# Optimization experiments

Measured on AMD Instinct MI355X. Metric: run time of the kernel, lower is better.

## Reference

```python
import jax, jax.numpy as jnp
import numpy as np

N_HEADS = 16
MAX_REL = 64  # max_relative_pos_len


def setup_inputs() -> dict:
    key = jax.random.key(0)
    ks = jax.random.split(key, 8)
    B, S, D = 2, 2048, 1024
    d = D // N_HEADS
    sc = 0.02
    return {
        "hidden_states": jax.random.normal(ks[0], (B, S, D), jnp.float32),
        "attention_mask": jnp.zeros((B, 1, 1, S), jnp.float32),
        "Wq": jax.random.normal(ks[1], (D, D), jnp.float32) * sc,
        "bq": jnp.zeros((D,), jnp.float32),
        "Wk": jax.random.normal(ks[2], (D, D), jnp.float32) * sc,
        "bk": jnp.zeros((D,), jnp.float32),
        "Wv": jax.random.normal(ks[3], (D, D), jnp.float32) * sc,
        "bv": jnp.zeros((D,), jnp.float32),
        "emb_k": jax.random.normal(ks[4], (2 * MAX_REL + 1, d), jnp.float32) * sc,
        "emb_v": jax.random.normal(ks[5], (2 * MAX_REL + 1, d), jnp.float32) * sc,
    }


def reference(hidden_states, attention_mask, Wq, bq, Wk, bk, Wv, bv, emb_k, emb_v):
    B, S, D = hidden_states.shape
    H = N_HEADS
    d = D // H
    scale = 1.0 / jnp.sqrt(jnp.asarray(d, hidden_states.dtype))

    def heads(x):  # [B,S,D] -> [B,H,S,d]
        return x.reshape(B, S, H, d).transpose(0, 2, 1, 3)

    q = heads(hidden_states @ Wq + bq)
    k = heads(hidden_states @ Wk + bk)
    v = heads(hidden_states @ Wv + bv)

    # relative position indices, clamped: [S_q, S_k]
    rel_idx = jnp.clip(jnp.arange(S)[:, None] - jnp.arange(S)[None, :], -MAX_REL, MAX_REL) + MAX_REL
    rel_k = emb_k[rel_idx]  # [S, S, d]

    # content scores + relative-key bias, both scaled by 1/sqrt(d)
    scores = (jnp.einsum('bhqd,bhkd->bhqk', q, k)
              + jnp.einsum('bhqd,qkd->bhqk', q, rel_k)) * scale
    scores = scores + attention_mask
    probs = jax.nn.softmax(scores, axis=-1)  # dropout is identity at p=0

    rel_v = emb_v[rel_idx]  # [S, S, d]
    ctx = (jnp.einsum('bhqk,bhkd->bhqd', probs, v)
           + jnp.einsum('bhqk,qkd->bhqd', probs, rel_v))
    return ctx.transpose(0, 2, 1, 3).reshape(B, S, D)
```

## Files before the change

kernel.cpp:

```cpp
#include <hip/hip_runtime.h>
#include <stdint.h>

typedef unsigned short u16;
typedef __attribute__((ext_vector_type(8))) short short8;
typedef __attribute__((ext_vector_type(4))) short s16x4;
typedef __attribute__((ext_vector_type(4))) float f32x4;
typedef __attribute__((ext_vector_type(4))) unsigned short u16x4;

#define S_LEN 2048
#define NH 16
#define DMODEL 1024
#define NR 129
#define LOG2E 1.44269504f

#define MFMA(a,b,c) __builtin_amdgcn_mfma_f32_16x16x32_bf16((a),(b),(c),0,0,0)

__device__ __forceinline__ u16 f2bf(float f){
  uint32_t u = __float_as_uint(f);
  u += 0x7fff + ((u >> 16) & 1);
  return (u16)(u >> 16);
}
__device__ __forceinline__ u16 f2bfa(float f){
  return (u16)((__float_as_uint(f) + 0x8000u) >> 16);
}
__device__ __forceinline__ float bf2f(u16 h){ return __uint_as_float(((uint32_t)h) << 16); }

__device__ __forceinline__ uint32_t cvtpk(float lo, float hi){
  uint32_t r;
  asm("v_cvt_pk_bf16_f32 %0, %1, %2" : "=v"(r) : "v"(lo), "v"(hi));
  return r;
}

__device__ __forceinline__ void gl_lds16(const u16* g, u16* l){
  __builtin_amdgcn_global_load_lds((const __attribute__((address_space(1))) void*)g,
                                   (__attribute__((address_space(3))) void*)l, 16, 0, 0);
}

__global__ __launch_bounds__(256) void k_prep(const float* __restrict__ X,
                                              const float* __restrict__ Wq, const float* __restrict__ Wk,
                                              const float* __restrict__ Wv, const float* __restrict__ Wemb,
                                              const float* __restrict__ mask,
                                              u16* __restrict__ Xb, u16* __restrict__ Wt,
                                              u16* __restrict__ Eb, float* __restrict__ maskL){
  const int bid = blockIdx.x, tid = threadIdx.x;
  if (bid < 4096){
    int i = bid * 256 + tid;
    const float4* xp = (const float4*)X;
    float4 v = xp[i];
    u16x4 o; o.x = f2bf(v.x); o.y = f2bf(v.y); o.z = f2bf(v.z); o.w = f2bf(v.w);
    *(u16x4*)(Xb + (size_t)i * 4) = o;
  } else if (bid < 4864){
    int b2 = bid - 4096;
    int z = b2 >> 8;
    const float* W = (z == 0) ? Wq : (z == 1) ? Wk : Wv;
    u16* Ot = Wt + (size_t)z * 1024 * 1024;
    __shared__ float t[64][65];
    int k0 = ((b2 >> 4) & 15) * 64, n0 = (b2 & 15) * 64;
    int c = tid & 63, r0 = (tid >> 6) * 16;
    #pragma unroll
    for (int i = 0; i < 16; ++i) t[r0 + i][c] = W[(size_t)(k0 + r0 + i) * 1024 + n0 + c];
    __syncthreads();
    #pragma unroll
    for (int i = 0; i < 16; ++i) Ot[(size_t)(n0 + r0 + i) * 1024 + k0 + c] = f2bf(t[c][r0 + i]);
  } else if (bid < 4900){
    int idx = (bid - 4864) * 256 + tid;
    if (idx < 144 * 64){
      int r = idx >> 6;
      Eb[idx] = (r < NR) ? f2bf(Wemb[idx]) : (u16)0;
    }
  } else {
    int idx = (bid - 4900) * 256 + tid;
    maskL[idx] = mask[idx] * LOG2E;
  }
}

__global__ __launch_bounds__(256) void k_qkv(const u16* __restrict__ Xb, const u16* __restrict__ Wt,
                                             const float* __restrict__ bq, const float* __restrict__ bk,
                                             const float* __restrict__ bv,
                                             u16* __restrict__ Qs, u16* __restrict__ Kb, u16* __restrict__ Vb){
  const int z = blockIdx.z;
  const u16* W = Wt + (size_t)z * 1024 * 1024;
  const float* bias = (z == 0) ? bq : (z == 1) ? bk : bv;
  u16* outp = (z == 0) ? Qs : (z == 1) ? Kb : Vb;
  const float vs = (z == 0) ? 0.125f * LOG2E : 1.0f;
  const int n0 = blockIdx.x * 128, m0 = blockIdx.y * 128;
  const int tid = threadIdx.x, w = tid >> 6, lane = tid & 63, l15 = lane & 15, quad = lane >> 4;
  const int wm = (w >> 1) * 64, wn = (w & 1) * 64;
  __shared__ __attribute__((aligned(16))) u16 As[128 * 32];
  __shared__ __attribute__((aligned(16))) u16 Bs[128 * 32];
  f32x4 acc[4][4];
  #pragma unroll
  for (int i = 0; i < 4; ++i)
    #pragma unroll
    for (int j = 0; j < 4; ++j) acc[i][j] = (f32x4){0.f,0.f,0.f,0.f};

  const int rA = lane >> 2, cA = (lane & 3) * 8;
  const u16* aBase = Xb + (size_t)(m0 + w * 16 + rA) * 1024 + cA;
  const u16* bBase = W  + (size_t)(n0 + w * 16 + rA) * 1024 + cA;
  u16* aDst0 = As + (w * 16) * 32;  u16* aDst1 = As + (64 + w * 16) * 32;
  u16* bDst0 = Bs + (w * 16) * 32;  u16* bDst1 = Bs + (64 + w * 16) * 32;

  for (int k0 = 0; k0 < 1024; k0 += 32){
    __syncthreads();
    gl_lds16(aBase + k0,             aDst0);
    gl_lds16(aBase + 64 * 1024 + k0, aDst1);
    gl_lds16(bBase + k0,             bDst0);
    gl_lds16(bBase + 64 * 1024 + k0, bDst1);
    __syncthreads();
    short8 af[4], bfr[4];
    #pragma unroll
    for (int f = 0; f < 4; ++f){
      af[f]  = *(const short8*)(As + (wm + f * 16 + l15) * 32 + quad * 8);
      bfr[f] = *(const short8*)(Bs + (wn + f * 16 + l15) * 32 + quad * 8);
    }
    #pragma unroll
    for (int i = 0; i < 4; ++i)
      #pragma unroll
      for (int j = 0; j < 4; ++j) acc[i][j] = MFMA(af[i], bfr[j], acc[i][j]);
  }
  #pragma unroll
  for (int i = 0; i < 4; ++i){
    #pragma unroll
    for (int j = 0; j < 4; ++j){
      int col = n0 + wn + j * 16 + l15;
      float bsv = bias[col];
      int hh = col >> 6, jd = col & 63;
      #pragma unroll
      for (int r = 0; r < 4; ++r){
        int row = m0 + wm + i * 16 + quad * 4 + r;
        int bb = row >> 11, s = row & 2047;
        float vv = (acc[i][j][r] + bsv) * vs;
        outp[(((size_t)(bb * 16 + hh)) * S_LEN + s) * 64 + jd] = f2bf(vv);
      }
    }
  }
}

__global__ __launch_bounds__(256) void k_transv(const u16* __restrict__ Vb, u16* __restrict__ Vt){
  const int g = blockIdx.y; const int s0 = blockIdx.x * 64;
  __shared__ __attribute__((aligned(16))) u16 t[64][72];
  const int tid = threadIdx.x;
  #pragma unroll
  for (int i = 0; i < 2; ++i){
    int c = tid + i * 256; int r = c >> 3, ch = (c & 7) * 8;
    *(short8*)&t[r][ch] = *(const short8*)(Vb + ((size_t)g * S_LEN + s0 + r) * 64 + ch);
  }
  __syncthreads();
  #pragma unroll
  for (int i = 0; i < 2; ++i){
    int c = tid + i * 256; int d = c >> 3, ch = (c & 7) * 8;
    short8 vv;
    #pragma unroll
    for (int u = 0; u < 8; ++u) vv[u] = (short)t[ch + u][d];
    *(short8*)(Vt + ((size_t)g * 64 + d) * S_LEN + s0 + ch) = vv;
  }
}

__global__ __launch_bounds__(256, 3) void k_flash(const u16* __restrict__ QS, const u16* __restrict__ KB,
                                                  const u16* __restrict__ VT, const u16* __restrict__ EMBK,
                                                  const float* __restrict__ maskL, const float* __restrict__ embv,
                                                  float* __restrict__ out){
  const int g = blockIdx.y; const int b = g >> 4; const int h = g & 15;
  const int q0 = blockIdx.x * 64;
  const int tid = threadIdx.x;
  const int w = tid >> 6; const int lane = tid & 63;
  const int l15 = lane & 15; const int quad = lane >> 4;
  const int wm = w * 16;
  const int rqb = quad * 4;
  const int qrow = q0 + wm + l15;

  __shared__ union UKE {
    struct {
      __attribute__((aligned(16))) u16 Ks[64][72];
      __attribute__((aligned(16))) u16 Vs[64][72];
    } s;
    __attribute__((aligned(16))) u16 Evs[64][136];
  } uu;
  __shared__ __attribute__((aligned(16))) u16 QEb[4][16][132];
  __shared__ __attribute__((aligned(16))) u16 Psb[64][136];

  {
    short8 z8 = (short8){0,0,0,0,0,0,0,0};
    for (int i = tid; i < 64 * 136 / 8; i += 256) ((short8*)Psb)[i] = z8;
  }

  const int srow0 = tid >> 3;
  const int srow1 = srow0 + 32;
  const int sch = (tid & 7) * 8;
  const int c0 = ((sch & 8) ? 32 : 0) + (sch >> 4) * 4;
  const u16* kSrc = KB + (size_t)g * S_LEN * 64 + sch;
  const u16* vSrc = VT + (size_t)g * 64 * S_LEN + sch;
  const float* mBase = maskL + b * S_LEN;

  short8 kr0 = *(const short8*)(kSrc + (size_t)srow0 * 64);
  short8 kr1 = *(const short8*)(kSrc + (size_t)srow1 * 64);
  short8 vr0 = *(const short8*)(vSrc + (size_t)srow0 * S_LEN);
  short8 vr1 = *(const short8*)(vSrc + (size_t)srow1 * S_LEN);
  f32x4 mcur[4];
  #pragma unroll
  for (int fn = 0; fn < 4; ++fn) mcur[fn] = *(const f32x4*)(mBase + fn * 16 + rqb);

  const u16* qptr = QS + ((size_t)g * S_LEN + q0 + wm + l15) * 64 + quad * 8;
  short8 qa0 = *(const short8*)qptr;
  short8 qa1 = *(const short8*)(qptr + 32);

  #pragma unroll
  for (int fn = 0; fn < 9; ++fn){
    const u16* ep = EMBK + (fn * 16 + l15) * 64 + quad * 8;
    short8 eb0 = *(const short8*)ep;
    short8 eb1 = *(const short8*)(ep + 32);
    f32x4 c = (f32x4){0.f,0.f,0.f,0.f};
    c = MFMA(qa0, eb0, c);
    c = MFMA(qa1, eb1, c);
    int col = fn * 16 + l15;
    if (col < NR){
      #pragma unroll
      for (int r = 0; r < 4; ++r) QEb[w][rqb + r][col] = f2bf(c[r]);
    }
  }
  __syncthreads();

  const float qeR = bf2f(QEb[w][l15][0]);
  const float qeL = bf2f(QEb[w][l15][128]);

  short8 bones;
  {
    short one = (l15 == 0) ? (short)0x3F80 : (short)0;
    #pragma unroll
    for (int j = 0; j < 8; ++j) bones[j] = one;
  }

  f32x4 o[4];
  #pragma unroll
  for (int f = 0; f < 4; ++f) o[f] = (f32x4){0.f,0.f,0.f,0.f};
  f32x4 lacc = (f32x4){0.f,0.f,0.f,0.f};
  float ll0v[4] = {0.f,0.f,0.f,0.f};
  float ll_mx = 0.f;
  float rsb_s = 0.f;

  for (int kt = 0; kt < S_LEN; kt += 64){
    __syncthreads();
    *(short8*)&uu.s.Ks[srow0][sch] = kr0;
    *(short8*)&uu.s.Ks[srow1][sch] = kr1;
    {
      s16x4 lo = __builtin_shufflevector(vr0, vr0, 0, 1, 2, 3);
      s16x4 hi = __builtin_shufflevector(vr0, vr0, 4, 5, 6, 7);
      *(s16x4*)&uu.s.Vs[srow0][c0]      = lo;
      *(s16x4*)&uu.s.Vs[srow0][c0 + 16] = hi;
    }
    {
      s16x4 lo = __builtin_shufflevector(vr1, vr1, 0, 1, 2, 3);
      s16x4 hi = __builtin_shufflevector(vr1, vr1, 4, 5, 6, 7);
      *(s16x4*)&uu.s.Vs[srow1][c0]      = lo;
      *(s16x4*)&uu.s.Vs[srow1][c0 + 16] = hi;
    }
    __syncthreads();

    const int ktn = kt + 64;
    f32x4 mnext[4];
    if (ktn < S_LEN){
      kr0 = *(const short8*)(kSrc + (size_t)(ktn + srow0) * 64);
      kr1 = *(const short8*)(kSrc + (size_t)(ktn + srow1) * 64);
      vr0 = *(const short8*)(vSrc + (size_t)srow0 * S_LEN + ktn);
      vr1 = *(const short8*)(vSrc + (size_t)srow1 * S_LEN + ktn);
      #pragma unroll
      for (int fn = 0; fn < 4; ++fn) mnext[fn] = *(const f32x4*)(mBase + ktn + fn * 16 + rqb);
    }

    const bool leftC  = (kt <= q0 - 128);
    const bool rightC = (kt >= q0 + 128);
    const float qeadd = leftC ? qeL : (rightC ? qeR : 0.f);

    f32x4 p4[4];
    __builtin_amdgcn_s_setprio(1);
    #pragma unroll
    for (int fn = 0; fn < 4; ++fn){
      short8 kb0 = *(const short8*)&uu.s.Ks[fn * 16 + l15][quad * 8];
      short8 kb1 = *(const short8*)&uu.s.Ks[fn * 16 + l15][32 + quad * 8];
      f32x4 c = mcur[fn] + qeadd;
      c = MFMA(kb0, qa0, c);
      c = MFMA(kb1, qa1, c);
      p4[fn] = c;
    }
    __builtin_amdgcn_s_setprio(0);

    if (leftC | rightC){
      #pragma unroll
      for (int fn = 0; fn < 4; ++fn)
        #pragma unroll
        for (int r = 0; r < 4; ++r) p4[fn][r] = __builtin_amdgcn_exp2f(p4[fn][r]);
    } else {
      #pragma unroll
      for (int fn = 0; fn < 4; ++fn){
        int kbase = kt + fn * 16 + rqb;
        #pragma unroll
        for (int r = 0; r < 4; ++r){
          int dq = qrow - (kbase + r) + 64;
          int ridx = min(max(dq, 0), 128);
          float p = __builtin_amdgcn_exp2f(p4[fn][r] + bf2f(QEb[w][l15][ridx]));
          ll_mx += (dq >= 128) ? p : 0.f;
          if (dq >= 1 && dq <= 127){
            Psb[wm + l15][127 - dq] = f2bfa(p);
            rsb_s += p;
          }
          p4[fn][r] = p;
        }
      }
    }

    __builtin_amdgcn_s_setprio(1);
    #pragma unroll
    for (int fp = 0; fp < 2; ++fp){
      union { uint32_t u[4]; short8 s8; } pk;
      pk.u[0] = cvtpk(p4[2 * fp][0],     p4[2 * fp][1]);
      pk.u[1] = cvtpk(p4[2 * fp][2],     p4[2 * fp][3]);
      pk.u[2] = cvtpk(p4[2 * fp + 1][0], p4[2 * fp + 1][1]);
      pk.u[3] = cvtpk(p4[2 * fp + 1][2], p4[2 * fp + 1][3]);
      short8 pa = pk.s8;
      lacc = MFMA(pa, bones, lacc);
      #pragma unroll
      for (int fd = 0; fd < 4; ++fd){
        short8 vb = *(const short8*)&uu.s.Vs[fd * 16 + l15][quad * 16 + fp * 8];
        o[fd] = MFMA(pa, vb, o[fd]);
      }
    }
    __builtin_amdgcn_s_setprio(0);

    if (kt == q0 - 128){
      #pragma unroll
      for (int r = 0; r < 4; ++r) ll0v[r] = lacc[r];
    }
    if (ktn < S_LEN){
      #pragma unroll
      for (int fn = 0; fn < 4; ++fn) mcur[fn] = mnext[fn];
    }
  }

  __syncthreads();
  {
    int d = tid & 63, t4 = tid >> 6;
    #pragma unroll
    for (int it = 0; it < 34; ++it){
      int t = t4 + it * 4;
      float v = (t <= 126) ? embv[(size_t)(127 - t) * 64 + d] : 0.f;
      uu.Evs[d][t] = f2bf(v);
    }
  }
  __syncthreads();

  f32x4 ob[4];
  #pragma unroll
  for (int f = 0; f < 4; ++f) ob[f] = (f32x4){0.f,0.f,0.f,0.f};
  #pragma unroll
  for (int kb = 0; kb < 4; ++kb){
    short8 pa = *(const short8*)&Psb[wm + l15][kb * 32 + quad * 8];
    #pragma unroll
    for (int fd = 0; fd < 4; ++fd){
      short8 vb = *(const short8*)&uu.Evs[fd * 16 + l15][kb * 32 + quad * 8];
      ob[fd] = MFMA(pa, vb, ob[fd]);
    }
  }

  #pragma unroll
  for (int st = 16; st < 64; st <<= 1){
    ll_mx += __shfl_xor(ll_mx, st, 64);
    rsb_s += __shfl_xor(rsb_s, st, 64);
  }

  float inv[4], tl[4], trr[4];
  #pragma unroll
  for (int r = 0; r < 4; ++r){
    float L   = __shfl(lacc[r], quad << 4);
    float l0  = __shfl(ll0v[r], quad << 4);
    int src   = (quad << 4) + rqb + r;
    float lmx = __shfl(ll_mx, src);
    float rv  = __shfl(rsb_s, src);
    inv[r] = 1.f / L;
    tl[r]  = (l0 + lmx) * inv[r];
    trr[r] = 1.f - tl[r] - rv * inv[r];
  }

  #pragma unroll
  for (int fd = 0; fd < 4; ++fd){
    int dim = fd * 16 + l15;
    float evL = embv[(size_t)128 * 64 + dim];
    float evR = embv[dim];
    #pragma unroll
    for (int r = 0; r < 4; ++r){
      int row = q0 + wm + rqb + r;
      float val = (o[fd][r] + ob[fd][r]) * inv[r] + tl[r] * evL + trr[r] * evR;
      out[((size_t)(b * S_LEN + row)) * DMODEL + h * 64 + dim] = val;
    }
  }
}

extern "C" void kernel_launch(void* const* d_in, const int* in_sizes, int n_in,
                              void* d_out, int out_size, void* d_ws, size_t ws_size,
                              hipStream_t stream){
  const float* X    = (const float*)d_in[0];
  const float* mask = (const float*)d_in[1];
  const float* Wq   = (const float*)d_in[2];
  const float* bq   = (const float*)d_in[3];
  const float* Wk   = (const float*)d_in[4];
  const float* bk   = (const float*)d_in[5];
  const float* Wv   = (const float*)d_in[6];
  const float* bv   = (const float*)d_in[7];
  const float* embk = (const float*)d_in[8];
  const float* embv = (const float*)d_in[9];
  float* out = (float*)d_out;
  char* ws = (char*)d_ws;

  u16* XB   = (u16*)(ws + 0);
  u16* WT   = (u16*)(ws + 8388608);
  u16* EKB  = (u16*)(ws + 14680064);
  u16* QS   = (u16*)(ws + 14698496);
  u16* KB   = (u16*)(ws + 23087104);
  u16* VB   = (u16*)(ws + 31475712);
  u16* VT   = (u16*)(ws + 39864320);
  float* MSL = (float*)(ws + 48252928);

  k_prep   <<<4916, 256, 0, stream>>>(X, Wq, Wk, Wv, embk, mask, XB, WT, EKB, MSL);
  k_qkv    <<<dim3(8, 32, 3), 256, 0, stream>>>(XB, WT, bq, bk, bv, QS, KB, VB);
  k_transv <<<dim3(32, 32), 256, 0, stream>>>(VB, VT);
  k_flash  <<<dim3(32, 32), 256, 0, stream>>>(QS, KB, VT, EKB, MSL, embv, out);
}
```

Before: 213.8 us.

## Write V transposed from QKV GEMM, load K fragments directly, double-buffer V

The QKV projection kernel now writes V directly in transposed [d,S] layout with 4-wide stores, which removes the separate transpose kernel and its launch. In the flash kernel, K fragments are loaded straight from global memory into registers instead of being staged through shared memory. V is double-buffered in an XOR-swizzled LDS layout, so each iteration needs only one barrier. QEb is moved into the union to save LDS. This trades more per-thread global K loads and register pressure for fewer barriers and less LDS traffic.

```diff
diff --git a/kernel.cpp b/kernel.cpp
--- a/kernel.cpp
+++ b/kernel.cpp
@@ -77,11 +77,10 @@
 __global__ __launch_bounds__(256) void k_qkv(const u16* __restrict__ Xb, const u16* __restrict__ Wt,
                                              const float* __restrict__ bq, const float* __restrict__ bk,
                                              const float* __restrict__ bv,
-                                             u16* __restrict__ Qs, u16* __restrict__ Kb, u16* __restrict__ Vb){
+                                             u16* __restrict__ Qs, u16* __restrict__ Kb, u16* __restrict__ Vt){
   const int z = blockIdx.z;
   const u16* W = Wt + (size_t)z * 1024 * 1024;
   const float* bias = (z == 0) ? bq : (z == 1) ? bk : bv;
-  u16* outp = (z == 0) ? Qs : (z == 1) ? Kb : Vb;
   const float vs = (z == 0) ? 0.125f * LOG2E : 1.0f;
   const int n0 = blockIdx.x * 128, m0 = blockIdx.y * 128;
   const int tid = threadIdx.x, w = tid >> 6, lane = tid & 63, l15 = lane & 15, quad = lane >> 4;
@@ -118,41 +117,41 @@
       #pragma unroll
       for (int j = 0; j < 4; ++j) acc[i][j] = MFMA(af[i], bfr[j], acc[i][j]);
   }
-  #pragma unroll
-  for (int i = 0; i < 4; ++i){
-    #pragma unroll
-    for (int j = 0; j < 4; ++j){
-      int col = n0 + wn + j * 16 + l15;
-      float bsv = bias[col];
-      int hh = col >> 6, jd = col & 63;
-      #pragma unroll
-      for (int r = 0; r < 4; ++r){
-        int row = m0 + wm + i * 16 + quad * 4 + r;
-        int bb = row >> 11, s = row & 2047;
-        float vv = (acc[i][j][r] + bsv) * vs;
-        outp[(((size_t)(bb * 16 + hh)) * S_LEN + s) * 64 + jd] = f2bf(vv);
-      }
-    }
-  }
-}
-
-__global__ __launch_bounds__(256) void k_transv(const u16* __restrict__ Vb, u16* __restrict__ Vt){
-  const int g = blockIdx.y; const int s0 = blockIdx.x * 64;
-  __shared__ __attribute__((aligned(16))) u16 t[64][72];
-  const int tid = threadIdx.x;
-  #pragma unroll
-  for (int i = 0; i < 2; ++i){
-    int c = tid + i * 256; int r = c >> 3, ch = (c & 7) * 8;
-    *(short8*)&t[r][ch] = *(const short8*)(Vb + ((size_t)g * S_LEN + s0 + r) * 64 + ch);
-  }
-  __syncthreads();
-  #pragma unroll
-  for (int i = 0; i < 2; ++i){
-    int c = tid + i * 256; int d = c >> 3, ch = (c & 7) * 8;
-    short8 vv;
-    #pragma unroll
-    for (int u = 0; u < 8; ++u) vv[u] = (short)t[ch + u][d];
-    *(short8*)(Vt + ((size_t)g * 64 + d) * S_LEN + s0 + ch) = vv;
+
+  if (z == 2){
+    #pragma unroll
+    for (int i = 0; i < 4; ++i){
+      int row0 = m0 + wm + i * 16 + quad * 4;
+      int bb = row0 >> 11, sb = row0 & 2047;
+      #pragma unroll
+      for (int j = 0; j < 4; ++j){
+        int col = n0 + wn + j * 16 + l15;
+        float bsv = bias[col];
+        int hh = col >> 6, jd = col & 63;
+        u16x4 vv;
+        #pragma unroll
+        for (int r = 0; r < 4; ++r) vv[r] = f2bf(acc[i][j][r] + bsv);
+        *(u16x4*)(Vt + ((size_t)(bb * 16 + hh) * 64 + jd) * S_LEN + sb) = vv;
+      }
+    }
+  } else {
+    u16* outp = (z == 0) ? Qs : Kb;
+    #pragma unroll
+    for (int i = 0; i < 4; ++i){
+      #pragma unroll
+      for (int j = 0; j < 4; ++j){
+        int col = n0 + wn + j * 16 + l15;
+        float bsv = bias[col];
+        int hh = col >> 6, jd = col & 63;
+        #pragma unroll
+        for (int r = 0; r < 4; ++r){
+          int row = m0 + wm + i * 16 + quad * 4 + r;
+          int bb = row >> 11, s = row & 2047;
+          float vv = (acc[i][j][r] + bsv) * vs;
+          outp[(((size_t)(bb * 16 + hh)) * S_LEN + s) * 64 + jd] = f2bf(vv);
+        }
+      }
+    }
   }
 }
 
@@ -171,12 +170,11 @@
 
   __shared__ union UKE {
     struct {
-      __attribute__((aligned(16))) u16 Ks[64][72];
-      __attribute__((aligned(16))) u16 Vs[64][72];
+      __attribute__((aligned(16))) u16 Vs[2][64][64];
+      __attribute__((aligned(16))) u16 QEb[4][16][132];
     } s;
     __attribute__((aligned(16))) u16 Evs[64][136];
   } uu;
-  __shared__ __attribute__((aligned(16))) u16 QEb[4][16][132];
   __shared__ __attribute__((aligned(16))) u16 Psb[64][136];
 
   {
@@ -187,15 +185,34 @@
   const int srow0 = tid >> 3;
   const int srow1 = srow0 + 32;
   const int sch = (tid & 7) * 8;
-  const int c0 = ((sch & 8) ? 32 : 0) + (sch >> 4) * 4;
-  const u16* kSrc = KB + (size_t)g * S_LEN * 64 + sch;
+  const int c0b = (((sch & 8) ? 32 : 0) + (sch >> 4) * 4) * 2;
+  const int off00 = srow0 * 128 + ((c0b)      ^ ((srow0 & 7) << 4));
+  const int off01 = srow0 * 128 + ((c0b + 32) ^ ((srow0 & 7) << 4));
+  const int off10 = srow1 * 128 + ((c0b)      ^ ((srow1 & 7) << 4));
+  const int off11 = srow1 * 128 + ((c0b + 32) ^ ((srow1 & 7) << 4));
   const u16* vSrc = VT + (size_t)g * 64 * S_LEN + sch;
   const float* mBase = maskL + b * S_LEN;
 
-  short8 kr0 = *(const short8*)(kSrc + (size_t)srow0 * 64);
-  short8 kr1 = *(const short8*)(kSrc + (size_t)srow1 * 64);
+  const u16* kfp = KB + ((size_t)g * S_LEN + l15) * 64 + quad * 8;
+  short8 kf[4][2];
+  #pragma unroll
+  for (int fn = 0; fn < 4; ++fn){
+    kf[fn][0] = *(const short8*)(kfp + (size_t)(fn * 16) * 64);
+    kf[fn][1] = *(const short8*)(kfp + (size_t)(fn * 16) * 64 + 32);
+  }
+
   short8 vr0 = *(const short8*)(vSrc + (size_t)srow0 * S_LEN);
   short8 vr1 = *(const short8*)(vSrc + (size_t)srow1 * S_LEN);
+  {
+    char* vb = (char*)uu.s.Vs[0];
+    *(s16x4*)(vb + off00) = __builtin_shufflevector(vr0, vr0, 0, 1, 2, 3);
+    *(s16x4*)(vb + off01) = __builtin_shufflevector(vr0, vr0, 4, 5, 6, 7);
+    *(s16x4*)(vb + off10) = __builtin_shufflevector(vr1, vr1, 0, 1, 2, 3);
+    *(s16x4*)(vb + off11) = __builtin_shufflevector(vr1, vr1, 4, 5, 6, 7);
+  }
+  vr0 = *(const short8*)(vSrc + (size_t)srow0 * S_LEN + 64);
+  vr1 = *(const short8*)(vSrc + (size_t)srow1 * S_LEN + 64);
+
   f32x4 mcur[4];
   #pragma unroll
   for (int fn = 0; fn < 4; ++fn) mcur[fn] = *(const f32x4*)(mBase + fn * 16 + rqb);
@@ -215,13 +232,13 @@
     int col = fn * 16 + l15;
     if (col < NR){
       #pragma unroll
-      for (int r = 0; r < 4; ++r) QEb[w][rqb + r][col] = f2bf(c[r]);
+      for (int r = 0; r < 4; ++r) uu.s.QEb[w][rqb + r][col] = f2bf(c[r]);
     }
   }
   __syncthreads();
 
-  const float qeR = bf2f(QEb[w][l15][0]);
-  const float qeL = bf2f(QEb[w][l15][128]);
+  const float qeR = bf2f(uu.s.QEb[w][l15][0]);
+  const float qeL = bf2f(uu.s.QEb[w][l15][128]);
 
   short8 bones;
   {
@@ -229,6 +246,11 @@
     #pragma unroll
     for (int j = 0; j < 8; ++j) bones[j] = one;
   }
+
+  const int vswz = (l15 & 7) << 4;
+  const int vrb  = l15 * 128;
+  const int vq0  = (quad * 32) ^ vswz;
+  const int vq1  = (quad * 32 + 16) ^ vswz;
 
   f32x4 o[4];
   #pragma unroll
@@ -238,33 +260,16 @@
   float ll_mx = 0.f;
   float rsb_s = 0.f;
 
+  int cur = 0;
   for (int kt = 0; kt < S_LEN; kt += 64){
-    __syncthreads();
-    *(short8*)&uu.s.Ks[srow0][sch] = kr0;
-    *(short8*)&uu.s.Ks[srow1][sch] = kr1;
+    const int ktn = kt + 64;
+
     {
-      s16x4 lo = __builtin_shufflevector(vr0, vr0, 0, 1, 2, 3);
-      s16x4 hi = __builtin_shufflevector(vr0, vr0, 4, 5, 6, 7);
-      *(s16x4*)&uu.s.Vs[srow0][c0]      = lo;
-      *(s16x4*)&uu.s.Vs[srow0][c0 + 16] = hi;
-    }
-    {
-      s16x4 lo = __builtin_shufflevector(vr1, vr1, 0, 1, 2, 3);
-      s16x4 hi = __builtin_shufflevector(vr1, vr1, 4, 5, 6, 7);
-      *(s16x4*)&uu.s.Vs[srow1][c0]      = lo;
-      *(s16x4*)&uu.s.Vs[srow1][c0 + 16] = hi;
-    }
-    __syncthreads();
-
-    const int ktn = kt + 64;
-    f32x4 mnext[4];
-    if (ktn < S_LEN){
-      kr0 = *(const short8*)(kSrc + (size_t)(ktn + srow0) * 64);
-      kr1 = *(const short8*)(kSrc + (size_t)(ktn + srow1) * 64);
-      vr0 = *(const short8*)(vSrc + (size_t)srow0 * S_LEN + ktn);
-      vr1 = *(const short8*)(vSrc + (size_t)srow1 * S_LEN + ktn);
-      #pragma unroll
-      for (int fn = 0; fn < 4; ++fn) mnext[fn] = *(const f32x4*)(mBase + ktn + fn * 16 + rqb);
+      char* vb = (char*)uu.s.Vs[cur ^ 1];
+      *(s16x4*)(vb + off00) = __builtin_shufflevector(vr0, vr0, 0, 1, 2, 3);
+      *(s16x4*)(vb + off01) = __builtin_shufflevector(vr0, vr0, 4, 5, 6, 7);
+      *(s16x4*)(vb + off10) = __builtin_shufflevector(vr1, vr1, 0, 1, 2, 3);
+      *(s16x4*)(vb + off11) = __builtin_shufflevector(vr1, vr1, 4, 5, 6, 7);
     }
 
     const bool leftC  = (kt <= q0 - 128);
@@ -275,14 +280,27 @@
     __builtin_amdgcn_s_setprio(1);
     #pragma unroll
     for (int fn = 0; fn < 4; ++fn){
-      short8 kb0 = *(const short8*)&uu.s.Ks[fn * 16 + l15][quad * 8];
-      short8 kb1 = *(const short8*)&uu.s.Ks[fn * 16 + l15][32 + quad * 8];
       f32x4 c = mcur[fn] + qeadd;
-      c = MFMA(kb0, qa0, c);
-      c = MFMA(kb1, qa1, c);
+      c = MFMA(kf[fn][0], qa0, c);
+      c = MFMA(kf[fn][1], qa1, c);
       p4[fn] = c;
     }
     __builtin_amdgcn_s_setprio(0);
+
+    f32x4 mnext[4];
+    if (ktn < S_LEN){
+      #pragma unroll
+      for (int fn = 0; fn < 4; ++fn){
+        kf[fn][0] = *(const short8*)(kfp + (size_t)(ktn + fn * 16) * 64);
+        kf[fn][1] = *(const short8*)(kfp + (size_t)(ktn + fn * 16) * 64 + 32);
+      }
+      #pragma unroll
+      for (int fn = 0; fn < 4; ++fn) mnext[fn] = *(const f32x4*)(mBase + ktn + fn * 16 + rqb);
+      if (kt + 128 < S_LEN){
+        vr0 = *(const short8*)(vSrc + (size_t)srow0 * S_LEN + kt + 128);
+        vr1 = *(const short8*)(vSrc + (size_t)srow1 * S_LEN + kt + 128);
+      }
+    }
 
     if (leftC | rightC){
       #pragma unroll
@@ -297,7 +315,7 @@
         for (int r = 0; r < 4; ++r){
           int dq = qrow - (kbase + r) + 64;
           int ridx = min(max(dq, 0), 128);
-          float p = __builtin_amdgcn_exp2f(p4[fn][r] + bf2f(QEb[w][l15][ridx]));
+          float p = __builtin_amdgcn_exp2f(p4[fn][r] + bf2f(uu.s.QEb[w][l15][ridx]));
           ll_mx += (dq >= 128) ? p : 0.f;
           if (dq >= 1 && dq <= 127){
             Psb[wm + l15][127 - dq] = f2bfa(p);
@@ -309,6 +327,7 @@
     }
 
     __builtin_amdgcn_s_setprio(1);
+    const char* vbase = (const char*)uu.s.Vs[cur];
     #pragma unroll
     for (int fp = 0; fp < 2; ++fp){
       union { uint32_t u[4]; short8 s8; } pk;
@@ -318,9 +337,10 @@
       pk.u[3] = cvtpk(p4[2 * fp + 1][2], p4[2 * fp + 1][3]);
       short8 pa = pk.s8;
       lacc = MFMA(pa, bones, lacc);
+      const int vq = fp ? vq1 : vq0;
       #pragma unroll
       for (int fd = 0; fd < 4; ++fd){
-        short8 vb = *(const short8*)&uu.s.Vs[fd * 16 + l15][quad * 16 + fp * 8];
+        short8 vb = *(const short8*)(vbase + fd * 2048 + vrb + vq);
         o[fd] = MFMA(pa, vb, o[fd]);
       }
     }
@@ -334,9 +354,10 @@
       #pragma unroll
       for (int fn = 0; fn < 4; ++fn) mcur[fn] = mnext[fn];
     }
-  }
-
-  __syncthreads();
+    __syncthreads();
+    cur ^= 1;
+  }
+
   {
     int d = tid & 63, t4 = tid >> 6;
     #pragma unroll
@@ -415,12 +436,10 @@
   u16* EKB  = (u16*)(ws + 14680064);
   u16* QS   = (u16*)(ws + 14698496);
   u16* KB   = (u16*)(ws + 23087104);
-  u16* VB   = (u16*)(ws + 31475712);
   u16* VT   = (u16*)(ws + 39864320);
   float* MSL = (float*)(ws + 48252928);
 
   k_prep   <<<4916, 256, 0, stream>>>(X, Wq, Wk, Wv, embk, mask, XB, WT, EKB, MSL);
-  k_qkv    <<<dim3(8, 32, 3), 256, 0, stream>>>(XB, WT, bq, bk, bv, QS, KB, VB);
-  k_transv <<<dim3(32, 32), 256, 0, stream>>>(VB, VT);
+  k_qkv    <<<dim3(8, 32, 3), 256, 0, stream>>>(XB, WT, bq, bk, bv, QS, KB, VT);
   k_flash  <<<dim3(32, 32), 256, 0, stream>>>(QS, KB, VT, EKB, MSL, embv, out);
 }
```

New measurement: 352.4 us. +64.8%, slower.

## Double-buffer K/V tiles via direct global-to-LDS loads with XOR-swizzled layout

Applied to the files above, without the earlier changes.

The flash kernel now streams K and V tiles straight from global memory into double-buffered shared memory. This replaces the register staging and the two barriers per iteration with one barrier per iteration. Shared arrays drop their padding and use an XOR swizzle to avoid bank conflicts, and the V transpose kernel writes a pre-permuted layout to match. The last relative-key column is kept in a register, QEb shrinks to 128 columns, and launch bounds drop to 2 waves per SIMD to make room for the larger LDS footprint, at the risk of lower occupancy.

```diff
diff --git a/kernel.cpp b/kernel.cpp
--- a/kernel.cpp
+++ b/kernel.cpp
@@ -3,7 +3,6 @@
 
 typedef unsigned short u16;
 typedef __attribute__((ext_vector_type(8))) short short8;
-typedef __attribute__((ext_vector_type(4))) short s16x4;
 typedef __attribute__((ext_vector_type(4))) float f32x4;
 typedef __attribute__((ext_vector_type(4))) unsigned short u16x4;
 
@@ -136,7 +135,7 @@
   }
 }
 
-__global__ __launch_bounds__(256) void k_transv(const u16* __restrict__ Vb, u16* __restrict__ Vt){
+__global__ __launch_bounds__(256) void k_transv(const u16* __restrict__ Vb, u16* __restrict__ Vp){
   const int g = blockIdx.y; const int s0 = blockIdx.x * 64;
   __shared__ __attribute__((aligned(16))) u16 t[64][72];
   const int tid = threadIdx.x;
@@ -149,15 +148,18 @@
   #pragma unroll
   for (int i = 0; i < 2; ++i){
     int c = tid + i * 256; int d = c >> 3, ch = (c & 7) * 8;
-    short8 vv;
-    #pragma unroll
-    for (int u = 0; u < 8; ++u) vv[u] = (short)t[ch + u][d];
-    *(short8*)(Vt + ((size_t)g * 64 + d) * S_LEN + s0 + ch) = vv;
-  }
-}
-
-__global__ __launch_bounds__(256, 3) void k_flash(const u16* __restrict__ QS, const u16* __restrict__ KB,
-                                                  const u16* __restrict__ VT, const u16* __restrict__ EMBK,
+    int q = (ch >> 2) & 3, f = ch >> 4;
+    u16x4 lo, hi;
+    #pragma unroll
+    for (int u = 0; u < 4; ++u){ lo[u] = t[ch + u][d]; hi[u] = t[ch + 4 + u][d]; }
+    u16* base = Vp + ((size_t)g * 64 + d) * S_LEN + s0;
+    *(u16x4*)(base + q * 16 + f * 4)       = lo;
+    *(u16x4*)(base + (q + 1) * 16 + f * 4) = hi;
+  }
+}
+
+__global__ __launch_bounds__(256, 2) void k_flash(const u16* __restrict__ QS, const u16* __restrict__ KB,
+                                                  const u16* __restrict__ VP, const u16* __restrict__ EMBK,
                                                   const float* __restrict__ maskL, const float* __restrict__ embv,
                                                   float* __restrict__ out){
   const int g = blockIdx.y; const int b = g >> 4; const int h = g & 15;
@@ -171,31 +173,34 @@
 
   __shared__ union UKE {
     struct {
-      __attribute__((aligned(16))) u16 Ks[64][72];
-      __attribute__((aligned(16))) u16 Vs[64][72];
+      __attribute__((aligned(16))) u16 K[2][4096];
+      __attribute__((aligned(16))) u16 V[2][4096];
     } s;
     __attribute__((aligned(16))) u16 Evs[64][136];
   } uu;
-  __shared__ __attribute__((aligned(16))) u16 QEb[4][16][132];
-  __shared__ __attribute__((aligned(16))) u16 Psb[64][136];
+  __shared__ __attribute__((aligned(16))) u16 QEb[4][16][128];
+  __shared__ __attribute__((aligned(16))) u16 Psb[64][128];
 
   {
     short8 z8 = (short8){0,0,0,0,0,0,0,0};
-    for (int i = tid; i < 64 * 136 / 8; i += 256) ((short8*)Psb)[i] = z8;
-  }
-
-  const int srow0 = tid >> 3;
-  const int srow1 = srow0 + 32;
-  const int sch = (tid & 7) * 8;
-  const int c0 = ((sch & 8) ? 32 : 0) + (sch >> 4) * 4;
-  const u16* kSrc = KB + (size_t)g * S_LEN * 64 + sch;
-  const u16* vSrc = VT + (size_t)g * 64 * S_LEN + sch;
+    for (int i = tid; i < 64 * 128 / 8; i += 256) ((short8*)Psb)[i] = z8;
+  }
+
+  const int lrow = lane >> 3;
+  const int lsw  = ((lane & 7) ^ lrow) * 8;
+  const u16* kS = KB + ((size_t)g * S_LEN + w * 16 + lrow) * 64 + lsw;
+  const u16* vS = VP + ((size_t)(g * 64 + w * 16 + lrow)) * S_LEN + lsw;
   const float* mBase = maskL + b * S_LEN;
 
-  short8 kr0 = *(const short8*)(kSrc + (size_t)srow0 * 64);
-  short8 kr1 = *(const short8*)(kSrc + (size_t)srow1 * 64);
-  short8 vr0 = *(const short8*)(vSrc + (size_t)srow0 * S_LEN);
-  short8 vr1 = *(const short8*)(vSrc + (size_t)srow1 * S_LEN);
+  {
+    u16* kd = uu.s.K[0] + (w * 16) * 64;
+    u16* vd = uu.s.V[0] + (w * 16) * 64;
+    gl_lds16(kS,               kd);
+    gl_lds16(kS + 8 * 64,      kd + 512);
+    gl_lds16(vS,               vd);
+    gl_lds16(vS + 8 * S_LEN,   vd + 512);
+  }
+
   f32x4 mcur[4];
   #pragma unroll
   for (int fn = 0; fn < 4; ++fn) mcur[fn] = *(const f32x4*)(mBase + fn * 16 + rqb);
@@ -204,6 +209,7 @@
   short8 qa0 = *(const short8*)qptr;
   short8 qa1 = *(const short8*)(qptr + 32);
 
+  float qeLf = 0.f;
   #pragma unroll
   for (int fn = 0; fn < 9; ++fn){
     const u16* ep = EMBK + (fn * 16 + l15) * 64 + quad * 8;
@@ -212,16 +218,24 @@
     f32x4 c = (f32x4){0.f,0.f,0.f,0.f};
     c = MFMA(qa0, eb0, c);
     c = MFMA(qa1, eb1, c);
-    int col = fn * 16 + l15;
-    if (col < NR){
-      #pragma unroll
-      for (int r = 0; r < 4; ++r) QEb[w][rqb + r][col] = f2bf(c[r]);
+    if (fn < 8){
+      #pragma unroll
+      for (int r = 0; r < 4; ++r) QEb[w][rqb + r][fn * 16 + l15] = f2bf(c[r]);
+    } else {
+      int srcl = (l15 >> 2) << 4;
+      float t0 = __shfl(c[0], srcl, 64);
+      float t1 = __shfl(c[1], srcl, 64);
+      float t2 = __shfl(c[2], srcl, 64);
+      float t3 = __shfl(c[3], srcl, 64);
+      int rr = l15 & 3;
+      float qv = (rr == 0) ? t0 : (rr == 1) ? t1 : (rr == 2) ? t2 : t3;
+      qeLf = bf2f(f2bf(qv));
     }
   }
   __syncthreads();
 
   const float qeR = bf2f(QEb[w][l15][0]);
-  const float qeL = bf2f(QEb[w][l15][128]);
+  const float qeL = qeLf;
 
   short8 bones;
   {
@@ -229,6 +243,12 @@
     #pragma unroll
     for (int j = 0; j < 8; ++j) bones[j] = one;
   }
+
+  const int rsw = l15 & 7;
+  const int kO0 = ((quad     ^ rsw) * 8);
+  const int kO1 = (((quad+4) ^ rsw) * 8);
+  const int vO0 = (((quad*2)     ^ rsw) * 8);
+  const int vO1 = (((quad*2 + 1) ^ rsw) * 8);
 
   f32x4 o[4];
   #pragma unroll
@@ -238,51 +258,43 @@
   float ll_mx = 0.f;
   float rsb_s = 0.f;
 
+  int cur = 0;
   for (int kt = 0; kt < S_LEN; kt += 64){
-    __syncthreads();
-    *(short8*)&uu.s.Ks[srow0][sch] = kr0;
-    *(short8*)&uu.s.Ks[srow1][sch] = kr1;
-    {
-      s16x4 lo = __builtin_shufflevector(vr0, vr0, 0, 1, 2, 3);
-      s16x4 hi = __builtin_shufflevector(vr0, vr0, 4, 5, 6, 7);
-      *(s16x4*)&uu.s.Vs[srow0][c0]      = lo;
-      *(s16x4*)&uu.s.Vs[srow0][c0 + 16] = hi;
-    }
-    {
-      s16x4 lo = __builtin_shufflevector(vr1, vr1, 0, 1, 2, 3);
-      s16x4 hi = __builtin_shufflevector(vr1, vr1, 4, 5, 6, 7);
-      *(s16x4*)&uu.s.Vs[srow1][c0]      = lo;
-      *(s16x4*)&uu.s.Vs[srow1][c0 + 16] = hi;
-    }
-    __syncthreads();
-
     const int ktn = kt + 64;
-    f32x4 mnext[4];
+
     if (ktn < S_LEN){
-      kr0 = *(const short8*)(kSrc + (size_t)(ktn + srow0) * 64);
-      kr1 = *(const short8*)(kSrc + (size_t)(ktn + srow1) * 64);
-      vr0 = *(const short8*)(vSrc + (size_t)srow0 * S_LEN + ktn);
-      vr1 = *(const short8*)(vSrc + (size_t)srow1 * S_LEN + ktn);
-      #pragma unroll
-      for (int fn = 0; fn < 4; ++fn) mnext[fn] = *(const f32x4*)(mBase + ktn + fn * 16 + rqb);
+      u16* kd = uu.s.K[cur ^ 1] + (w * 16) * 64;
+      u16* vd = uu.s.V[cur ^ 1] + (w * 16) * 64;
+      gl_lds16(kS + (size_t)ktn * 64,        kd);
+      gl_lds16(kS + (size_t)(ktn + 8) * 64,  kd + 512);
+      gl_lds16(vS + ktn,                     vd);
+      gl_lds16(vS + ktn + 8 * S_LEN,         vd + 512);
     }
 
     const bool leftC  = (kt <= q0 - 128);
     const bool rightC = (kt >= q0 + 128);
     const float qeadd = leftC ? qeL : (rightC ? qeR : 0.f);
 
+    const u16* ks = uu.s.K[cur];
     f32x4 p4[4];
     __builtin_amdgcn_s_setprio(1);
     #pragma unroll
     for (int fn = 0; fn < 4; ++fn){
-      short8 kb0 = *(const short8*)&uu.s.Ks[fn * 16 + l15][quad * 8];
-      short8 kb1 = *(const short8*)&uu.s.Ks[fn * 16 + l15][32 + quad * 8];
+      const u16* krow = ks + (fn * 16 + l15) * 64;
+      short8 kb0 = *(const short8*)(krow + kO0);
+      short8 kb1 = *(const short8*)(krow + kO1);
       f32x4 c = mcur[fn] + qeadd;
       c = MFMA(kb0, qa0, c);
       c = MFMA(kb1, qa1, c);
       p4[fn] = c;
     }
     __builtin_amdgcn_s_setprio(0);
+
+    f32x4 mnext[4];
+    if (ktn < S_LEN){
+      #pragma unroll
+      for (int fn = 0; fn < 4; ++fn) mnext[fn] = *(const f32x4*)(mBase + ktn + fn * 16 + rqb);
+    }
 
     if (leftC | rightC){
       #pragma unroll
@@ -296,11 +308,13 @@
         #pragma unroll
         for (int r = 0; r < 4; ++r){
           int dq = qrow - (kbase + r) + 64;
-          int ridx = min(max(dq, 0), 128);
-          float p = __builtin_amdgcn_exp2f(p4[fn][r] + bf2f(QEb[w][l15][ridx]));
+          int ridx = min(max(dq, 0), 127);
+          float qv = (dq >= 128) ? qeL : bf2f(QEb[w][l15][ridx]);
+          float p = __builtin_amdgcn_exp2f(p4[fn][r] + qv);
           ll_mx += (dq >= 128) ? p : 0.f;
           if (dq >= 1 && dq <= 127){
-            Psb[wm + l15][127 - dq] = f2bfa(p);
+            int t = 127 - dq;
+            Psb[wm + l15][(((t >> 3) ^ rsw) << 3) | (t & 7)] = f2bfa(p);
             rsb_s += p;
           }
           p4[fn][r] = p;
@@ -309,6 +323,7 @@
     }
 
     __builtin_amdgcn_s_setprio(1);
+    const u16* vs = uu.s.V[cur];
     #pragma unroll
     for (int fp = 0; fp < 2; ++fp){
       union { uint32_t u[4]; short8 s8; } pk;
@@ -318,9 +333,10 @@
       pk.u[3] = cvtpk(p4[2 * fp + 1][2], p4[2 * fp + 1][3]);
       short8 pa = pk.s8;
       lacc = MFMA(pa, bones, lacc);
+      const int vO = fp ? vO1 : vO0;
       #pragma unroll
       for (int fd = 0; fd < 4; ++fd){
-        short8 vb = *(const short8*)&uu.s.Vs[fd * 16 + l15][quad * 16 + fp * 8];
+        short8 vb = *(const short8*)(vs + (fd * 16 + l15) * 64 + vO);
         o[fd] = MFMA(pa, vb, o[fd]);
       }
     }
@@ -334,9 +350,10 @@
       #pragma unroll
       for (int fn = 0; fn < 4; ++fn) mcur[fn] = mnext[fn];
     }
-  }
-
-  __syncthreads();
+    __syncthreads();
+    cur ^= 1;
+  }
+
   {
     int d = tid & 63, t4 = tid >> 6;
     #pragma unroll
@@ -353,7 +370,7 @@
   for (int f = 0; f < 4; ++f) ob[f] = (f32x4){0.f,0.f,0.f,0.f};
   #pragma unroll
   for (int kb = 0; kb < 4; ++kb){
-    short8 pa = *(const short8*)&Psb[wm + l15][kb * 32 + quad * 8];
+    short8 pa = *(const short8*)&Psb[wm + l15][((kb * 4 + quad) ^ rsw) << 3];
     #pragma unroll
     for (int fd = 0; fd < 4; ++fd){
       short8 vb = *(const short8*)&uu.Evs[fd * 16 + l15][kb * 32 + quad * 8];
@@ -416,11 +433,11 @@
   u16* QS   = (u16*)(ws + 14698496);
   u16* KB   = (u16*)(ws + 23087104);
   u16* VB   = (u16*)(ws + 31475712);
-  u16* VT   = (u16*)(ws + 39864320);
+  u16* VP   = (u16*)(ws + 39864320);
   float* MSL = (float*)(ws + 48252928);
 
   k_prep   <<<4916, 256, 0, stream>>>(X, Wq, Wk, Wv, embk, mask, XB, WT, EKB, MSL);
   k_qkv    <<<dim3(8, 32, 3), 256, 0, stream>>>(XB, WT, bq, bk, bv, QS, KB, VB);
-  k_transv <<<dim3(32, 32), 256, 0, stream>>>(VB, VT);
-  k_flash  <<<dim3(32, 32), 256, 0, stream>>>(QS, KB, VT, EKB, MSL, embv, out);
-}
+  k_transv <<<dim3(32, 32), 256, 0, stream>>>(VB, VP);
+  k_flash  <<<dim3(32, 32), 256, 0, stream>>>(QS, KB, VP, EKB, MSL, embv, out);
+}
```

New measurement: 223.7 us. 4.6% more time.
